# Optimization experiments

Hardware: AMD Instinct MI355X
Metric: run time of the kernel (lower is better)

## Reference

```python
import jax, jax.numpy as jnp
import numpy as np

IN_FEATURES = 256
OUT_FEATURES = 128
ALPHA = 0.2  # LeakyReLU negative slope
NEG_INF = -9e15
N_NODES = 8192


def _xavier_uniform(key, shape, gain):
    fan_in, fan_out = shape[0], shape[1]
    limit = gain * np.sqrt(6.0 / (fan_in + fan_out))
    return jax.random.uniform(key, shape, jnp.float32, -limit, limit)


def setup_inputs() -> dict:
    key = jax.random.key(0)
    k_h, k_adj, k_W, k_a = jax.random.split(key, 4)
    h = jax.random.normal(k_h, (N_NODES, IN_FEATURES), dtype=jnp.float32)
    adj = jax.random.randint(k_adj, (N_NODES, N_NODES), 0, 2, dtype=jnp.int32)
    W = _xavier_uniform(k_W, (IN_FEATURES, OUT_FEATURES), gain=1.414)
    a = _xavier_uniform(k_a, (2 * OUT_FEATURES, 1), gain=1.414)
    return {"h": h, "adj": adj, "W": W, "a": a}


def reference(h, adj, W, a):
    # Wh: (N, F_out)
    Wh = h @ W
    # Decompose a = [a1; a2]; e_ij = leakyrelu(Wh_i . a1 + Wh_j . a2)
    # == the original concat([Wh_i, Wh_j]) @ a, without the O(N^2*2F) tensor.
    a1 = a[:OUT_FEATURES, 0]  # (F_out,)
    a2 = a[OUT_FEATURES:, 0]  # (F_out,)
    src = Wh @ a1  # (N,)
    dst = Wh @ a2  # (N,)
    e = jax.nn.leaky_relu(src[:, None] + dst[None, :], negative_slope=ALPHA)  # (N, N)
    attention = jnp.where(adj > 0, e, NEG_INF)
    attention = jax.nn.softmax(attention, axis=1)
    # dropout p=0.0 (eval) -> identity
    h_prime = attention @ Wh  # (N, F_out)
    return jax.nn.elu(h_prime)  # concat=True
```

## Files before the change

### kernel.cpp

```cpp
#include <hip/hip_runtime.h>

#define N_NODES 8192
#define IN_F    256
#define OUT_F   128
#define ALPHA_S 0.2f

typedef __attribute__((ext_vector_type(8))) short  short8;
typedef __attribute__((ext_vector_type(4))) short  short4v;
typedef __attribute__((ext_vector_type(4))) float  floatx4;
typedef __attribute__((ext_vector_type(4))) int    intx4;
typedef __attribute__((ext_vector_type(4))) float  fx4;

static __device__ __forceinline__ short f2bf(float f) {
    union { float f; unsigned int i; } u; u.f = f;
    unsigned int r = u.i + 0x7FFFu + ((u.i >> 16) & 1u);
    return (short)(r >> 16);
}
static __device__ __forceinline__ float bf2f(short s) {
    union { float f; unsigned int i; } u;
    u.i = ((unsigned int)(unsigned short)s) << 16;
    return u.f;
}

__global__ __launch_bounds__(512) void k_wh(
    const float* __restrict__ h,
    const float* __restrict__ W,
    const float* __restrict__ a,
    short* __restrict__ WhT,
    float* __restrict__ src,
    float* __restrict__ dst)
{
    __shared__ short Wt[OUT_F][IN_F + 8];
    __shared__ short htile[32][IN_F + 8];
    __shared__ float q1s[IN_F], q2s[IN_F];
    __shared__ short wh_t[OUT_F][40];

    const int t      = threadIdx.x;
    const int lane   = t & 63;
    const int wave   = t >> 6;
    const int r_base = blockIdx.x * 32;

#pragma unroll
    for (int rep = 0; rep < 4; ++rep) {
        const int idx = rep * 8192 + t * 16;
        const int k   = idx >> 7;
        const int f   = idx & 127;
        fx4 w0 = *(const fx4*)(W + idx);
        fx4 w1 = *(const fx4*)(W + idx + 4);
        fx4 w2 = *(const fx4*)(W + idx + 8);
        fx4 w3 = *(const fx4*)(W + idx + 12);
        fx4 a10 = *(const fx4*)(a + f);
        fx4 a11 = *(const fx4*)(a + f + 4);
        fx4 a12 = *(const fx4*)(a + f + 8);
        fx4 a13 = *(const fx4*)(a + f + 12);
        fx4 a20 = *(const fx4*)(a + OUT_F + f);
        fx4 a21 = *(const fx4*)(a + OUT_F + f + 4);
        fx4 a22 = *(const fx4*)(a + OUT_F + f + 8);
        fx4 a23 = *(const fx4*)(a + OUT_F + f + 12);
        float p1 = 0.f, p2 = 0.f;
#pragma unroll
        for (int e = 0; e < 4; ++e) {
            p1 = fmaf(w0[e], a10[e], p1); p2 = fmaf(w0[e], a20[e], p2);
            p1 = fmaf(w1[e], a11[e], p1); p2 = fmaf(w1[e], a21[e], p2);
            p1 = fmaf(w2[e], a12[e], p1); p2 = fmaf(w2[e], a22[e], p2);
            p1 = fmaf(w3[e], a13[e], p1); p2 = fmaf(w3[e], a23[e], p2);
        }
#pragma unroll
        for (int e = 0; e < 4; ++e) {
            Wt[f + e][k]      = f2bf(w0[e]);
            Wt[f + 4 + e][k]  = f2bf(w1[e]);
            Wt[f + 8 + e][k]  = f2bf(w2[e]);
            Wt[f + 12 + e][k] = f2bf(w3[e]);
        }
#pragma unroll
        for (int m = 1; m < 8; m <<= 1) {
            p1 += __shfl_xor(p1, m, 64);
            p2 += __shfl_xor(p2, m, 64);
        }
        if ((t & 7) == 0) { q1s[k] = p1; q2s[k] = p2; }
    }

    const int r0   = t >> 4;
    const int fgrp = t & 15;
    const int k0   = fgrp * 16;
    fx4 h0, h1, h2, h3;
    {
        const float* hp = h + (size_t)(r_base + r0) * IN_F + k0;
        h0 = *(const fx4*)hp; h1 = *(const fx4*)(hp + 4);
        h2 = *(const fx4*)(hp + 8); h3 = *(const fx4*)(hp + 12);
        short8 b0, b1;
#pragma unroll
        for (int e = 0; e < 4; ++e) {
            b0[e]     = f2bf(h0[e]); b0[4 + e] = f2bf(h1[e]);
            b1[e]     = f2bf(h2[e]); b1[4 + e] = f2bf(h3[e]);
        }
        *(short8*)&htile[r0][k0]     = b0;
        *(short8*)&htile[r0][k0 + 8] = b1;
    }
    __syncthreads();

    {
        float sp = 0.f, dp = 0.f;
#pragma unroll
        for (int e = 0; e < 4; ++e) {
            sp = fmaf(h0[e], q1s[k0 + e], sp);      dp = fmaf(h0[e], q2s[k0 + e], dp);
            sp = fmaf(h1[e], q1s[k0 + 4 + e], sp);  dp = fmaf(h1[e], q2s[k0 + 4 + e], dp);
            sp = fmaf(h2[e], q1s[k0 + 8 + e], sp);  dp = fmaf(h2[e], q2s[k0 + 8 + e], dp);
            sp = fmaf(h3[e], q1s[k0 + 12 + e], sp); dp = fmaf(h3[e], q2s[k0 + 12 + e], dp);
        }
#pragma unroll
        for (int m = 1; m < 16; m <<= 1) {
            sp += __shfl_xor(sp, m, 64);
            dp += __shfl_xor(dp, m, 64);
        }
        if (fgrp == 0) { src[r_base + r0] = sp; dst[r_base + r0] = dp; }
    }

    const int ln15 = lane & 15;
    const int q    = lane >> 4;
    const int f0   = wave * 16;
    floatx4 c0 = {0.f, 0.f, 0.f, 0.f};
    floatx4 c1 = {0.f, 0.f, 0.f, 0.f};
#pragma unroll
    for (int s = 0; s < 8; ++s) {
        short8 bf  = *(const short8*)&Wt[f0 + ln15][s * 32 + q * 8];
        short8 a0f = *(const short8*)&htile[ln15][s * 32 + q * 8];
        short8 a1f = *(const short8*)&htile[16 + ln15][s * 32 + q * 8];
        c0 = __builtin_amdgcn_mfma_f32_16x16x32_bf16(a0f, bf, c0, 0, 0, 0);
        c1 = __builtin_amdgcn_mfma_f32_16x16x32_bf16(a1f, bf, c1, 0, 0, 0);
    }
    {
        short4v p0, p1;
#pragma unroll
        for (int r = 0; r < 4; ++r) { p0[r] = f2bf(c0[r]); p1[r] = f2bf(c1[r]); }
        *(short4v*)&wh_t[f0 + ln15][q * 4]      = p0;
        *(short4v*)&wh_t[f0 + ln15][16 + q * 4] = p1;
    }
    __syncthreads();
    {
        const int f    = t >> 2;
        const int half = t & 3;
        *(short8*)(WhT + (size_t)f * N_NODES + r_base + half * 8) =
            *(const short8*)&wh_t[f][half * 8];
    }
}

#define BM 16
#define BK 256
#define WPAD (BK + 8)
#define NIT (N_NODES / BK)

__global__ __launch_bounds__(512, 4) void k_attn(
    const int*   __restrict__ adj,
    const short* __restrict__ WhT,
    const float* __restrict__ src,
    const float* __restrict__ dstv,
    float* __restrict__ out)
{
    __shared__ short wbuf[2][BM * WPAD];
    __shared__ float denom_acc[BM];

    const int t    = threadIdx.x;
    const int lane = t & 63;
    const int wave = t >> 6;
    const int r0   = blockIdx.x * BM;

    const int sm  = t >> 5;
    const int sk0 = (t & 31) * 8;
    const float srow = src[r0 + sm];
    const int*   abase = adj  + (size_t)(r0 + sm) * N_NODES + sk0;
    const float* dbase = dstv + sk0;

    const int ln15 = lane & 15;
    const int q    = lane >> 4;
    const int f0   = wave * 16;
    const short* bbase = WhT + (size_t)(f0 + ln15) * N_NODES + q * 8;

    if ((t & 31) == 0) denom_acc[sm] = 0.f;

    floatx4 acc = {0.f, 0.f, 0.f, 0.f};

    intx4 mA0 = *(const intx4*)abase;
    intx4 mA1 = *(const intx4*)(abase + 4);
    fx4   dA0 = *(const fx4*)dbase;
    fx4   dA1 = *(const fx4*)(dbase + 4);
    intx4 mB0 = *(const intx4*)(abase + BK);
    intx4 mB1 = *(const intx4*)(abase + BK + 4);
    fx4   dB0 = *(const fx4*)(dbase + BK);
    fx4   dB1 = *(const fx4*)(dbase + BK + 4);

#define ATTN_STEP(IT, P, M0, M1, D0, D1)                                      \
    {                                                                         \
        short8 wv;                                                            \
        float rsum = 0.f;                                                     \
        _Pragma("unroll") for (int e = 0; e < 4; ++e) {                       \
            float x = srow + D0[e];                                           \
            float l = fmaxf(x, ALPHA_S * x);                                  \
            short b = (M0[e] > 0) ? f2bf(__expf(l)) : (short)0;               \
            wv[e] = b; rsum += bf2f(b);                                       \
        }                                                                     \
        _Pragma("unroll") for (int e = 0; e < 4; ++e) {                       \
            float x = srow + D1[e];                                           \
            float l = fmaxf(x, ALPHA_S * x);                                  \
            short b = (M1[e] > 0) ? f2bf(__expf(l)) : (short)0;               \
            wv[4 + e] = b; rsum += bf2f(b);                                   \
        }                                                                     \
        *(short8*)&wbuf[P][sm * WPAD + sk0] = wv;                             \
        _Pragma("unroll") for (int m = 1; m < 32; m <<= 1)                    \
            rsum += __shfl_xor(rsum, m, 64);                                  \
        if ((t & 31) == 0) denom_acc[sm] += rsum;                             \
        if ((IT) + 2 < NIT) {                                                 \
            const int o = ((IT) + 2) * BK;                                    \
            M0 = *(const intx4*)(abase + o);                                  \
            M1 = *(const intx4*)(abase + o + 4);                              \
            D0 = *(const fx4*)(dbase + o);                                    \
            D1 = *(const fx4*)(dbase + o + 4);                                \
        }                                                                     \
        short8 bfr[8];                                                        \
        const short* bb = bbase + (IT) * BK;                                  \
        _Pragma("unroll") for (int ks = 0; ks < 8; ++ks)                      \
            bfr[ks] = *(const short8*)(bb + ks * 32);                         \
        asm volatile("s_waitcnt lgkmcnt(0)" ::: "memory");                    \
        __builtin_amdgcn_s_barrier();                                         \
        asm volatile("" ::: "memory");                                        \
        const short* ab = &wbuf[P][ln15 * WPAD + q * 8];                      \
        _Pragma("unroll") for (int ks = 0; ks < 8; ++ks) {                    \
            short8 afr = *(const short8*)(ab + ks * 32);                      \
            acc = __builtin_amdgcn_mfma_f32_16x16x32_bf16(afr, bfr[ks], acc,  \
                                                          0, 0, 0);           \
        }                                                                     \
    }

    for (int it = 0; it < NIT; it += 2) {
        ATTN_STEP(it,     0, mA0, mA1, dA0, dA1)
        ATTN_STEP(it + 1, 1, mB0, mB1, dB0, dB1)
    }
#undef ATTN_STEP

    __syncthreads();

    float* op = out + (size_t)r0 * OUT_F + f0 + ln15;
#pragma unroll
    for (int r = 0; r < 4; ++r) {
        float dn = denom_acc[q * 4 + r];
        float v  = acc[r];
        v = (dn != 0.f) ? (v / dn) : 0.f;
        v = v > 0.f ? v : (__expf(v) - 1.f);
        op[(size_t)(q * 4 + r) * OUT_F] = v;
    }
}

extern "C" void kernel_launch(void* const* d_in, const int* in_sizes, int n_in,
                              void* d_out, int out_size, void* d_ws, size_t ws_size,
                              hipStream_t stream) {
    const float* h   = (const float*)d_in[0];
    const int*   adj = (const int*)d_in[1];
    const float* W   = (const float*)d_in[2];
    const float* a   = (const float*)d_in[3];
    float* out = (float*)d_out;

    char*  ws  = (char*)d_ws;
    short* WhT = (short*)ws;
    float* src = (float*)(ws + (2 << 20));
    float* dst = src + N_NODES;

    k_wh  <<<256, 512, 0, stream>>>(h, W, a, WhT, src, dst);
    k_attn<<<512, 512, 0, stream>>>(adj, WhT, src, dst, out);
}
```

Baseline: 426.3 us.

## Double attention block to 1024 threads with split-K MFMA and per-wave row denominators

Each attention block now runs 16 waves instead of 8. Each wave handles one adjacency row for the exp and mask phase, so the row sum reduces across the full wave in a register rather than through shared-memory atomics. The MFMA phase is split along K: two groups of 8 waves each cover half of the 256-wide tile, and their partial accumulators are combined through shared memory at the end. The intent is more memory-level parallelism per block and fewer per-wave global WhT loads. The costs are larger blocks, heavier register pressure from launch_bounds(1024,8), and an extra reduction step.

```diff
diff --git a/kernel.cpp b/kernel.cpp
--- a/kernel.cpp
+++ b/kernel.cpp
@@ -150,7 +150,7 @@
 #define WPAD (BK + 8)
 #define NIT (N_NODES / BK)
 
-__global__ __launch_bounds__(512, 4) void k_attn(
+__global__ __launch_bounds__(1024, 8) void k_attn(
     const int*   __restrict__ adj,
     const short* __restrict__ WhT,
     const float* __restrict__ src,
@@ -158,95 +158,95 @@
     float* __restrict__ out)
 {
     __shared__ short wbuf[2][BM * WPAD];
-    __shared__ float denom_acc[BM];
+    __shared__ float denom_s[BM];
 
     const int t    = threadIdx.x;
     const int lane = t & 63;
     const int wave = t >> 6;
     const int r0   = blockIdx.x * BM;
 
-    const int sm  = t >> 5;
-    const int sk0 = (t & 31) * 8;
+    const int sm  = wave;
+    const int sk0 = lane * 4;
     const float srow = src[r0 + sm];
     const int*   abase = adj  + (size_t)(r0 + sm) * N_NODES + sk0;
     const float* dbase = dstv + sk0;
 
     const int ln15 = lane & 15;
     const int q    = lane >> 4;
-    const int f0   = wave * 16;
-    const short* bbase = WhT + (size_t)(f0 + ln15) * N_NODES + q * 8;
-
-    if ((t & 31) == 0) denom_acc[sm] = 0.f;
+    const int f0   = (wave & 7) * 16;
+    const int koff = (wave >> 3) * 128;
+    const short* bbase = WhT + (size_t)(f0 + ln15) * N_NODES + koff + q * 8;
 
     floatx4 acc = {0.f, 0.f, 0.f, 0.f};
-
-    intx4 mA0 = *(const intx4*)abase;
-    intx4 mA1 = *(const intx4*)(abase + 4);
-    fx4   dA0 = *(const fx4*)dbase;
-    fx4   dA1 = *(const fx4*)(dbase + 4);
-    intx4 mB0 = *(const intx4*)(abase + BK);
-    intx4 mB1 = *(const intx4*)(abase + BK + 4);
-    fx4   dB0 = *(const fx4*)(dbase + BK);
-    fx4   dB1 = *(const fx4*)(dbase + BK + 4);
-
-#define ATTN_STEP(IT, P, M0, M1, D0, D1)                                      \
+    float dreg = 0.f;
+
+    intx4 mA = *(const intx4*)abase;
+    fx4   dA = *(const fx4*)dbase;
+    intx4 mB = *(const intx4*)(abase + BK);
+    fx4   dB = *(const fx4*)(dbase + BK);
+
+#define ATTN_STEP(IT, P, M, D)                                                \
     {                                                                         \
-        short8 wv;                                                            \
+        short4v wv;                                                           \
         float rsum = 0.f;                                                     \
         _Pragma("unroll") for (int e = 0; e < 4; ++e) {                       \
-            float x = srow + D0[e];                                           \
+            float x = srow + D[e];                                            \
             float l = fmaxf(x, ALPHA_S * x);                                  \
-            short b = (M0[e] > 0) ? f2bf(__expf(l)) : (short)0;               \
+            short b = (M[e] > 0) ? f2bf(__expf(l)) : (short)0;                \
             wv[e] = b; rsum += bf2f(b);                                       \
         }                                                                     \
-        _Pragma("unroll") for (int e = 0; e < 4; ++e) {                       \
-            float x = srow + D1[e];                                           \
-            float l = fmaxf(x, ALPHA_S * x);                                  \
-            short b = (M1[e] > 0) ? f2bf(__expf(l)) : (short)0;               \
-            wv[4 + e] = b; rsum += bf2f(b);                                   \
+        *(short4v*)&wbuf[P][sm * WPAD + sk0] = wv;                            \
+        _Pragma("unroll") for (int m = 1; m < 64; m <<= 1)                    \
+            rsum += __shfl_xor(rsum, m, 64);                                  \
+        dreg += rsum;                                                         \
+        if ((IT) + 2 < NIT) {                                                 \
+            M = *(const intx4*)(abase + ((IT) + 2) * BK);                     \
+            D = *(const fx4*)(dbase + ((IT) + 2) * BK);                       \
         }                                                                     \
-        *(short8*)&wbuf[P][sm * WPAD + sk0] = wv;                             \
-        _Pragma("unroll") for (int m = 1; m < 32; m <<= 1)                    \
-            rsum += __shfl_xor(rsum, m, 64);                                  \
-        if ((t & 31) == 0) denom_acc[sm] += rsum;                             \
-        if ((IT) + 2 < NIT) {                                                 \
-            const int o = ((IT) + 2) * BK;                                    \
-            M0 = *(const intx4*)(abase + o);                                  \
-            M1 = *(const intx4*)(abase + o + 4);                              \
-            D0 = *(const fx4*)(dbase + o);                                    \
-            D1 = *(const fx4*)(dbase + o + 4);                                \
-        }                                                                     \
-        short8 bfr[8];                                                        \
         const short* bb = bbase + (IT) * BK;                                  \
-        _Pragma("unroll") for (int ks = 0; ks < 8; ++ks)                      \
-            bfr[ks] = *(const short8*)(bb + ks * 32);                         \
+        short8 bfr0 = *(const short8*)(bb);                                   \
+        short8 bfr1 = *(const short8*)(bb + 32);                              \
+        short8 bfr2 = *(const short8*)(bb + 64);                              \
+        short8 bfr3 = *(const short8*)(bb + 96);                              \
         asm volatile("s_waitcnt lgkmcnt(0)" ::: "memory");                    \
         __builtin_amdgcn_s_barrier();                                         \
         asm volatile("" ::: "memory");                                        \
-        const short* ab = &wbuf[P][ln15 * WPAD + q * 8];                      \
-        _Pragma("unroll") for (int ks = 0; ks < 8; ++ks) {                    \
-            short8 afr = *(const short8*)(ab + ks * 32);                      \
-            acc = __builtin_amdgcn_mfma_f32_16x16x32_bf16(afr, bfr[ks], acc,  \
-                                                          0, 0, 0);           \
-        }                                                                     \
+        const short* ab = &wbuf[P][ln15 * WPAD + koff + q * 8];               \
+        short8 a0 = *(const short8*)(ab);                                     \
+        short8 a1 = *(const short8*)(ab + 32);                                \
+        short8 a2 = *(const short8*)(ab + 64);                                \
+        short8 a3 = *(const short8*)(ab + 96);                                \
+        acc = __builtin_amdgcn_mfma_f32_16x16x32_bf16(a0, bfr0, acc, 0, 0, 0);\
+        acc = __builtin_amdgcn_mfma_f32_16x16x32_bf16(a1, bfr1, acc, 0, 0, 0);\
+        acc = __builtin_amdgcn_mfma_f32_16x16x32_bf16(a2, bfr2, acc, 0, 0, 0);\
+        acc = __builtin_amdgcn_mfma_f32_16x16x32_bf16(a3, bfr3, acc, 0, 0, 0);\
     }
 
     for (int it = 0; it < NIT; it += 2) {
-        ATTN_STEP(it,     0, mA0, mA1, dA0, dA1)
-        ATTN_STEP(it + 1, 1, mB0, mB1, dB0, dB1)
+        ATTN_STEP(it,     0, mA, dA)
+        ATTN_STEP(it + 1, 1, mB, dB)
     }
 #undef ATTN_STEP
 
+    if (lane == 0) denom_s[sm] = dreg;
+    float* red = (float*)&wbuf[0][0];
+    if (wave >= 8) {
+#pragma unroll
+        for (int r = 0; r < 4; ++r)
+            red[(wave & 7) * 256 + (q * 4 + r) * 16 + ln15] = acc[r];
+    }
     __syncthreads();
 
-    float* op = out + (size_t)r0 * OUT_F + f0 + ln15;
-#pragma unroll
-    for (int r = 0; r < 4; ++r) {
-        float dn = denom_acc[q * 4 + r];
-        float v  = acc[r];
-        v = (dn != 0.f) ? (v / dn) : 0.f;
-        v = v > 0.f ? v : (__expf(v) - 1.f);
-        op[(size_t)(q * 4 + r) * OUT_F] = v;
+    if (wave < 8) {
+        float* op = out + (size_t)r0 * OUT_F + f0 + ln15;
+#pragma unroll
+        for (int r = 0; r < 4; ++r) {
+            float dn = denom_s[q * 4 + r];
+            float v  = acc[r] + red[wave * 256 + (q * 4 + r) * 16 + ln15];
+            v = (dn != 0.f) ? (v / dn) : 0.f;
+            v = v > 0.f ? v : (__expf(v) - 1.f);
+            op[(size_t)(q * 4 + r) * OUT_F] = v;
+        }
     }
 }
 
@@ -264,6 +264,6 @@
     float* src = (float*)(ws + (2 << 20));
     float* dst = src + N_NODES;
 
-    k_wh  <<<256, 512, 0, stream>>>(h, W, a, WhT, src, dst);
-    k_attn<<<512, 512, 0, stream>>>(adj, WhT, src, dst, out);
-}
+    k_wh  <<<256,  512, 0, stream>>>(h, W, a, WhT, src, dst);
+    k_attn<<<512, 1024, 0, stream>>>(adj, WhT, src, dst, out);
+}
```

Result: slower. 459.6 us (+7.8%).
